# Kernel optimization log

Measured on AMD Instinct MI355X. Metric: run time of the kernel, lower is better.

The kernel has to match this reference:

```python
import jax, jax.numpy as jnp
import numpy as np

DIM = 128
N = 8192
E = 262144
EPS = 1e-8  # torch.cosine_similarity eps


def setup_inputs() -> dict:
    key = jax.random.key(0)
    k1, k2, k3, k4 = jax.random.split(key, 4)
    x = jax.random.normal(k1, (N, DIM), dtype=jnp.float32)
    edge_index = jax.random.randint(k2, (2, E), 0, N, dtype=jnp.int32)
    # GCNConv parameters: linear weight (glorot-ish) and bias
    W_gcn = jax.random.normal(k3, (DIM, DIM), dtype=jnp.float32) / np.sqrt(DIM)
    b_gcn = jnp.zeros((DIM,), dtype=jnp.float32)
    return {"x": x, "edge_index": edge_index, "W_gcn": W_gcn, "b_gcn": b_gcn}


def _cosine_attention(x):
    # torch.cosine_similarity(x.unsqueeze(1), x.unsqueeze(0), dim=-1)
    # == (x @ x.T) / max(||x_i|| * ||x_j||, eps)
    nrm = jnp.sqrt(jnp.sum(x * x, axis=-1))                      # [N]
    denom = jnp.maximum(nrm[:, None] * nrm[None, :], EPS)        # [N, N]
    sim = (x @ x.T) / denom                                      # [N, N]
    return jax.nn.sigmoid(sim @ x)                               # [N, dim]


def _gcn_conv(x, edge_index, W, b):
    n = x.shape[0]
    xw = x @ W                                                   # [N, dim]
    # add self-loops
    loops = jnp.arange(n, dtype=edge_index.dtype)
    row = jnp.concatenate([edge_index[0], loops])                # source
    col = jnp.concatenate([edge_index[1], loops])                # target
    # symmetric normalization: deg computed on target nodes
    deg = jax.ops.segment_sum(jnp.ones_like(col, dtype=x.dtype), col, num_segments=n)
    dis = jnp.where(deg > 0, jax.lax.rsqrt(jnp.maximum(deg, 1.0)), 0.0)
    dis = jnp.where(deg > 0, deg ** -0.5, 0.0)
    norm = dis[row] * dis[col]                                   # [E+N]
    msgs = xw[row] * norm[:, None]                               # [E+N, dim]
    out = jax.ops.segment_sum(msgs, col, num_segments=n)         # [N, dim]
    return out + b


def reference(x, edge_index, W_gcn, b_gcn):
    att = _cosine_attention(x)
    g = _gcn_conv(x, edge_index, W_gcn, b_gcn)
    return g * att
```

## Files before the change

### kernel.cpp

```cpp
#include <hip/hip_runtime.h>
#include <math.h>

#define NN   8192
#define DIM  128
#define NE   262144
#define XB   128
#define HB   64
#define EPB  (NE / HB)
#define RWB  32
#define BK   16
#define SMEMF (64 * DIM + 64)

static __device__ __forceinline__ unsigned short f2bf(float f) {
  unsigned int u = __float_as_uint(f);
  return (unsigned short)((u + 0x7FFFu + ((u >> 16) & 1u)) >> 16);
}
static __device__ __forceinline__ float bf2f(unsigned short h) {
  return __uint_as_float((unsigned int)h << 16);
}


static __device__ void ph_xtx(int u, int tid, float* smem,
    const float* __restrict__ x, float* __restrict__ rinv,
    float* __restrict__ Mpart) {
  float* xs  = smem;
  float* rvs = smem + 64 * DIM;
  int row0 = u * 64;
  const float4* xsrc = (const float4*)(x + (size_t)row0 * DIM);
  float4* xdst = (float4*)xs;
  #pragma unroll
  for (int i = 0; i < 8; ++i) xdst[tid + 256 * i] = xsrc[tid + 256 * i];
  __syncthreads();
  int rr = tid >> 2, q = tid & 3;
  const float4* xr = (const float4*)&xs[rr * DIM + q * 32];
  float ss = 0.f;
  #pragma unroll
  for (int i = 0; i < 8; ++i) {
    float4 v = xr[i];
    ss += v.x * v.x + v.y * v.y + v.z * v.z + v.w * v.w;
  }
  ss += __shfl_xor(ss, 1);
  ss += __shfl_xor(ss, 2);
  if (q == 0) { float rv = 1.0f / sqrtf(ss); rvs[rr] = rv; rinv[row0 + rr] = rv; }
  __syncthreads();

  int ty = tid >> 4, tx = tid & 15;
  float acc[8][8];
  #pragma unroll
  for (int i = 0; i < 8; ++i)
    #pragma unroll
    for (int j = 0; j < 8; ++j) acc[i][j] = 0.f;
  #pragma unroll 2
  for (int r = 0; r < 64; ++r) {
    float4 a0 = *(const float4*)&xs[r * DIM + ty * 8];
    float4 a1 = *(const float4*)&xs[r * DIM + ty * 8 + 4];
    float4 b0 = *(const float4*)&xs[r * DIM + tx * 8];
    float4 b1 = *(const float4*)&xs[r * DIM + tx * 8 + 4];
    float rv = rvs[r];
    float a[8] = {a0.x * rv, a0.y * rv, a0.z * rv, a0.w * rv,
                  a1.x * rv, a1.y * rv, a1.z * rv, a1.w * rv};
    float b[8] = {b0.x, b0.y, b0.z, b0.w, b1.x, b1.y, b1.z, b1.w};
    #pragma unroll
    for (int i = 0; i < 8; ++i)
      #pragma unroll
      for (int j = 0; j < 8; ++j) acc[i][j] += a[i] * b[j];
  }
  float* o = Mpart + (size_t)u * (DIM * DIM);
  #pragma unroll
  for (int i = 0; i < 8; ++i) {
    *(float4*)&o[(ty * 8 + i) * DIM + tx * 8]     = make_float4(acc[i][0], acc[i][1], acc[i][2], acc[i][3]);
    *(float4*)&o[(ty * 8 + i) * DIM + tx * 8 + 4] = make_float4(acc[i][4], acc[i][5], acc[i][6], acc[i][7]);
  }
}

static __device__ void ph_hist(int h, int tid, int* ldeg,
    const int* __restrict__ ei, int* __restrict__ gcnt, int* __restrict__ slot) {
  int4* lz = (int4*)ldeg;
  #pragma unroll
  for (int i = tid; i < NN / 4; i += 256) lz[i] = make_int4(0, 0, 0, 0);
  __syncthreads();
  int e0 = h * EPB + tid * 16;
  int4 c0 = *(const int4*)(ei + NE + e0);
  int4 c1 = *(const int4*)(ei + NE + e0 + 4);
  int4 c2 = *(const int4*)(ei + NE + e0 + 8);
  int4 c3 = *(const int4*)(ei + NE + e0 + 12);
  int r0  = atomicAdd(&ldeg[c0.x], 1);
  int r1  = atomicAdd(&ldeg[c0.y], 1);
  int r2  = atomicAdd(&ldeg[c0.z], 1);
  int r3  = atomicAdd(&ldeg[c0.w], 1);
  int r4  = atomicAdd(&ldeg[c1.x], 1);
  int r5  = atomicAdd(&ldeg[c1.y], 1);
  int r6  = atomicAdd(&ldeg[c1.z], 1);
  int r7  = atomicAdd(&ldeg[c1.w], 1);
  int r8  = atomicAdd(&ldeg[c2.x], 1);
  int r9  = atomicAdd(&ldeg[c2.y], 1);
  int r10 = atomicAdd(&ldeg[c2.z], 1);
  int r11 = atomicAdd(&ldeg[c2.w], 1);
  int r12 = atomicAdd(&ldeg[c3.x], 1);
  int r13 = atomicAdd(&ldeg[c3.y], 1);
  int r14 = atomicAdd(&ldeg[c3.z], 1);
  int r15 = atomicAdd(&ldeg[c3.w], 1);
  __syncthreads();
  int binb = tid * 32;
  #pragma unroll
  for (int i = 0; i < 8; ++i) {
    int4 v = *(int4*)&ldeg[binb + i * 4];
    if (v.x) ldeg[binb + i * 4 + 0] = atomicAdd(&gcnt[binb + i * 4 + 0], v.x);
    if (v.y) ldeg[binb + i * 4 + 1] = atomicAdd(&gcnt[binb + i * 4 + 1], v.y);
    if (v.z) ldeg[binb + i * 4 + 2] = atomicAdd(&gcnt[binb + i * 4 + 2], v.z);
    if (v.w) ldeg[binb + i * 4 + 3] = atomicAdd(&gcnt[binb + i * 4 + 3], v.w);
  }
  __syncthreads();
  int4 s0 = make_int4(ldeg[c0.x] + r0,  ldeg[c0.y] + r1,  ldeg[c0.z] + r2,  ldeg[c0.w] + r3);
  int4 s1 = make_int4(ldeg[c1.x] + r4,  ldeg[c1.y] + r5,  ldeg[c1.z] + r6,  ldeg[c1.w] + r7);
  int4 s2 = make_int4(ldeg[c2.x] + r8,  ldeg[c2.y] + r9,  ldeg[c2.z] + r10, ldeg[c2.w] + r11);
  int4 s3 = make_int4(ldeg[c3.x] + r12, ldeg[c3.y] + r13, ldeg[c3.z] + r14, ldeg[c3.w] + r15);
  *(int4*)(slot + e0)      = s0;
  *(int4*)(slot + e0 + 4)  = s1;
  *(int4*)(slot + e0 + 8)  = s2;
  *(int4*)(slot + e0 + 12) = s3;
}

static __device__ void ph_mred(int u, int tid, float* smem,
    const float* __restrict__ Mpart, float* __restrict__ Mmat) {
  int j0 = u * 64;
  int jj = tid & 63, sub = tid >> 6;
  const float* mp = Mpart + (size_t)(sub * 32) * (DIM * DIM) + j0;
  float s = 0.f;
  #pragma unroll 4
  for (int k = 0; k < 32; ++k) s += mp[(size_t)k * (DIM * DIM) + jj];
  smem[sub * 64 + jj] = s;
  __syncthreads();
  if (tid < 64)
    Mmat[j0 + tid] = smem[tid] + smem[64 + tid] + smem[128 + tid] + smem[192 + tid];
}

static __device__ void ph_scan(int tid, int* wsum,
    const int* __restrict__ gcnt, int* __restrict__ offs, float* __restrict__ dis) {
  int lane = tid & 63, wave = tid >> 6;
  const int4* g4 = (const int4*)gcnt;
  int s = 0;
  #pragma unroll
  for (int i = 0; i < 8; ++i) { int4 v = g4[tid * 8 + i]; s += v.x + v.y + v.z + v.w; }
  int sc = s;
  #pragma unroll
  for (int off = 1; off < 64; off <<= 1) {
    int v = __shfl_up(sc, off);
    if (lane >= off) sc += v;
  }
  if (lane == 63) wsum[wave] = sc;
  __syncthreads();
  if (wave == 0 && lane < 4) {
    int v = wsum[lane];
    #pragma unroll
    for (int off = 1; off < 4; off <<= 1) {
      int u = __shfl_up(v, off);
      if (lane >= off) v += u;
    }
    wsum[lane] = v;
  }
  __syncthreads();
  int run = (wave ? wsum[wave - 1] : 0) + sc - s;
  #pragma unroll
  for (int i = 0; i < 8; ++i) {
    int4 v = g4[tid * 8 + i];
    int4 o;
    o.x = run; run += v.x;
    o.y = run; run += v.y;
    o.z = run; run += v.z;
    o.w = run; run += v.w;
    *(int4*)&offs[tid * 32 + i * 4] = o;
    float4 d;
    d.x = rsqrtf((float)(v.x + 1)); d.y = rsqrtf((float)(v.y + 1));
    d.z = rsqrtf((float)(v.z + 1)); d.w = rsqrtf((float)(v.w + 1));
    *(float4*)&dis[tid * 32 + i * 4] = d;
  }
}

static __device__ void ph_gemm(int u, int tid, float* smem,
    const float* __restrict__ x, const float* __restrict__ W,
    const float* __restrict__ Mmat, const float* __restrict__ rinv,
    const float* __restrict__ dis, unsigned short* __restrict__ xws,
    float* __restrict__ att) {
  float* xs  = smem;
  float* Wl  = smem + 4096;
  float* Ml  = smem + 6144;
  float* rvs = smem + 8192;
  float* dss = smem + 8224;
  int row0 = u * RWB;
  const float4* xsrc = (const float4*)(x + (size_t)row0 * DIM);
  float4* xdst = (float4*)xs;
  #pragma unroll
  for (int i = 0; i < 4; ++i) xdst[tid + 256 * i] = xsrc[tid + 256 * i];
  if (tid < RWB) { rvs[tid] = rinv[row0 + tid]; dss[tid] = dis[row0 + tid]; }

  int ty = tid >> 5, tx = tid & 31;
  int r0 = ty * 4;
  float4 aw[4], am[4];
  #pragma unroll
  for (int j = 0; j < 4; ++j) { aw[j] = make_float4(0,0,0,0); am[j] = make_float4(0,0,0,0); }

  for (int kk = 0; kk < DIM; kk += BK) {
    __syncthreads();
    const float4* Ws = (const float4*)(W + (size_t)kk * DIM);
    const float4* Ms = (const float4*)(Mmat + (size_t)kk * DIM);
    float4 w0s = Ws[tid], w1s = Ws[tid + 256];
    float4 m0s = Ms[tid], m1s = Ms[tid + 256];
    ((float4*)Wl)[tid]       = w0s;
    ((float4*)Wl)[tid + 256] = w1s;
    ((float4*)Ml)[tid]       = m0s;
    ((float4*)Ml)[tid + 256] = m1s;
    __syncthreads();
    #pragma unroll
    for (int k4 = 0; k4 < BK; k4 += 4) {
      float4 xf[4];
      #pragma unroll
      for (int j = 0; j < 4; ++j)
        xf[j] = *(const float4*)&xs[(r0 + j) * DIM + kk + k4];
      #pragma unroll
      for (int k = 0; k < 4; ++k) {
        float4 wv = *(const float4*)&Wl[(k4 + k) * DIM + tx * 4];
        float4 mv = *(const float4*)&Ml[(k4 + k) * DIM + tx * 4];
        #pragma unroll
        for (int j = 0; j < 4; ++j) {
          float xv = ((const float*)&xf[j])[k];
          aw[j].x += xv * wv.x; aw[j].y += xv * wv.y;
          aw[j].z += xv * wv.z; aw[j].w += xv * wv.w;
          am[j].x += xv * mv.x; am[j].y += xv * mv.y;
          am[j].z += xv * mv.z; am[j].w += xv * mv.w;
        }
      }
    }
  }
  #pragma unroll
  for (int j = 0; j < 4; ++j) {
    int row = row0 + r0 + j;
    float rv = rvs[r0 + j], ds = dss[r0 + j];
    size_t o = (size_t)row * DIM + tx * 4;
    ushort4 wb;
    wb.x = f2bf(aw[j].x * ds);
    wb.y = f2bf(aw[j].y * ds);
    wb.z = f2bf(aw[j].z * ds);
    wb.w = f2bf(aw[j].w * ds);
    *(ushort4*)&xws[o] = wb;
    float4 g;
    g.x = 1.0f / (1.0f + __expf(-am[j].x * rv));
    g.y = 1.0f / (1.0f + __expf(-am[j].y * rv));
    g.z = 1.0f / (1.0f + __expf(-am[j].z * rv));
    g.w = 1.0f / (1.0f + __expf(-am[j].w * rv));
    *(float4*)&att[o] = g;
  }
}

static __device__ void ph_place(int u, int tid,
    const int* __restrict__ ei, const int* __restrict__ offs,
    const int* __restrict__ slot, int* __restrict__ sorted) {
  int e0 = u * EPB + tid * 16;
  #pragma unroll
  for (int i = 0; i < 4; ++i) {
    int4 sv = *(const int4*)(ei + e0 + i * 4);
    int4 cv = *(const int4*)(ei + NE + e0 + i * 4);
    int4 sl = *(const int4*)(slot + e0 + i * 4);
    sorted[offs[cv.x] + sl.x] = sv.x;
    sorted[offs[cv.y] + sl.y] = sv.y;
    sorted[offs[cv.z] + sl.z] = sv.z;
    sorted[offs[cv.w] + sl.w] = sv.w;
  }
}

__global__ __launch_bounds__(256) void k_pA(const float* __restrict__ x,
    const int* __restrict__ ei, float* __restrict__ rinv,
    float* __restrict__ Mpart, int* __restrict__ gcnt, int* __restrict__ slot) {
  __shared__ float smem[SMEMF];
  int u = blockIdx.x, tid = threadIdx.x;
  if (u < XB) ph_xtx(u, tid, smem, x, rinv, Mpart);
  else        ph_hist(u - XB, tid, (int*)smem, ei, gcnt, slot);
}
__global__ __launch_bounds__(256) void k_pB(const float* __restrict__ Mpart,
    float* __restrict__ Mmat, const int* __restrict__ gcnt,
    int* __restrict__ offs, float* __restrict__ dis) {
  __shared__ float smem[SMEMF];
  int u = blockIdx.x, tid = threadIdx.x;
  if (u < 256) ph_mred(u, tid, smem, Mpart, Mmat);
  else         ph_scan(tid, (int*)smem, gcnt, offs, dis);
}
__global__ __launch_bounds__(256) void k_pC(const float* __restrict__ x,
    const float* __restrict__ W, const float* __restrict__ Mmat,
    const float* __restrict__ rinv, const float* __restrict__ dis,
    const int* __restrict__ ei, const int* __restrict__ offs,
    const int* __restrict__ slot, int* __restrict__ sorted,
    unsigned short* __restrict__ xws, float* __restrict__ att) {
  __shared__ float smem[SMEMF];
  int u = blockIdx.x, tid = threadIdx.x;
  if (u < NN / RWB) ph_gemm(u, tid, smem, x, W, Mmat, rinv, dis, xws, att);
  else              ph_place(u - NN / RWB, tid, ei, offs, slot, sorted);
}
__global__ __launch_bounds__(128) void k_pD(const int* __restrict__ offs,
    const int* __restrict__ gcnt, const float* __restrict__ dis,
    const unsigned short* __restrict__ xws, const float* __restrict__ att,
    const float* __restrict__ bias, const int* __restrict__ sorted,
    float* __restrict__ out) {
  int c = blockIdx.x, t = threadIdx.x;
  int base = offs[c];
  int cnt  = gcnt[c];
  float acc = bf2f(xws[(size_t)c * DIM + t]);
  int k = 0;
  for (; k + 4 <= cnt; k += 4) {
    int s0 = sorted[base + k + 0];
    int s1 = sorted[base + k + 1];
    int s2 = sorted[base + k + 2];
    int s3 = sorted[base + k + 3];
    float v0 = bf2f(xws[(size_t)s0 * DIM + t]);
    float v1 = bf2f(xws[(size_t)s1 * DIM + t]);
    float v2 = bf2f(xws[(size_t)s2 * DIM + t]);
    float v3 = bf2f(xws[(size_t)s3 * DIM + t]);
    acc += v0 + v1 + v2 + v3;
  }
  for (; k < cnt; ++k)
    acc += bf2f(xws[(size_t)sorted[base + k] * DIM + t]);
  float g = acc * dis[c] + bias[t];
  out[(size_t)c * DIM + t] = g * att[(size_t)c * DIM + t];
}

extern "C" void kernel_launch(void* const* d_in, const int* in_sizes, int n_in,
                              void* d_out, int out_size, void* d_ws, size_t ws_size,
                              hipStream_t stream) {
  const float* x  = (const float*)d_in[0];
  const int*   ei = (const int*)  d_in[1];
  const float* W  = (const float*)d_in[2];
  const float* b  = (const float*)d_in[3];
  float* out = (float*)d_out;

  unsigned short* xws = (unsigned short*)d_ws;
  float* att   = (float*)(xws + (size_t)NN * DIM);
  float* Mpart = att + (size_t)NN * DIM;
  float* Mmat  = Mpart + (size_t)XB * DIM * DIM;
  float* rinv  = Mmat + DIM * DIM;
  float* dis   = rinv + NN;
  int*   gcnt  = (int*)(dis + NN);
  int*   offs  = gcnt + NN;
  int*   slot  = offs + NN;
  int*   sorted= slot + NE;

  hipMemsetAsync(gcnt, 0, NN * sizeof(int), stream);

  k_pA<<<XB + HB, 256, 0, stream>>>(x, ei, rinv, Mpart, gcnt, slot);
  k_pB<<<257, 256, 0, stream>>>(Mpart, Mmat, gcnt, offs, dis);
  k_pC<<<NN / RWB + HB, 256, 0, stream>>>(x, W, Mmat, rinv, dis, ei, offs,
                                          slot, sorted, xws, att);
  k_pD<<<NN, 128, 0, stream>>>(offs, gcnt, dis, xws, att, b, sorted, out);
}
```

Measured before the change: 117.5 us.

## Rework GEMM thread tiling, pad smem, and vectorize bf16 gather in aggregation

The Gram-matrix phase switches to a split-half column mapping that cuts LDS bank conflicts. The fused GEMM now runs 128 threads per block, each holding an 8-column tile, and stores x in padded shared memory. The place phase uses more, smaller blocks. The aggregation kernel drops to 64 threads per node and reads two bf16 values per 32-bit load, with int4 index loads and an 8-way unroll. Together these aim to raise memory efficiency and ILP in the gather-heavy final kernel, at the cost of fewer threads per block and more registers.

Result: no change. 116.4 us (-0.9%).

```diff
diff --git a/kernel.cpp b/kernel.cpp
--- a/kernel.cpp
+++ b/kernel.cpp
@@ -5,18 +5,21 @@
 #define DIM  128
 #define NE   262144
 #define XB   128
-#define HB   64
-#define EPB  (NE / HB)
+#define HBH  64
+#define HEB  (NE / HBH)
+#define PBP  128
+#define PEB  (NE / PBP)
 #define RWB  32
 #define BK   16
-#define SMEMF (64 * DIM + 64)
+#define XSS  132
+#define SMEMF 8448
 
 static __device__ __forceinline__ unsigned short f2bf(float f) {
   unsigned int u = __float_as_uint(f);
   return (unsigned short)((u + 0x7FFFu + ((u >> 16) & 1u)) >> 16);
 }
-static __device__ __forceinline__ float bf2f(unsigned short h) {
-  return __uint_as_float((unsigned int)h << 16);
+static __device__ __forceinline__ float bf2f(unsigned int h) {
+  return __uint_as_float(h << 16);
 }
 
 
@@ -52,10 +55,10 @@
     for (int j = 0; j < 8; ++j) acc[i][j] = 0.f;
   #pragma unroll 2
   for (int r = 0; r < 64; ++r) {
-    float4 a0 = *(const float4*)&xs[r * DIM + ty * 8];
-    float4 a1 = *(const float4*)&xs[r * DIM + ty * 8 + 4];
-    float4 b0 = *(const float4*)&xs[r * DIM + tx * 8];
-    float4 b1 = *(const float4*)&xs[r * DIM + tx * 8 + 4];
+    float4 a0 = *(const float4*)&xs[r * DIM + ty * 4];
+    float4 a1 = *(const float4*)&xs[r * DIM + 64 + ty * 4];
+    float4 b0 = *(const float4*)&xs[r * DIM + tx * 4];
+    float4 b1 = *(const float4*)&xs[r * DIM + 64 + tx * 4];
     float rv = rvs[r];
     float a[8] = {a0.x * rv, a0.y * rv, a0.z * rv, a0.w * rv,
                   a1.x * rv, a1.y * rv, a1.z * rv, a1.w * rv};
@@ -68,8 +71,9 @@
   float* o = Mpart + (size_t)u * (DIM * DIM);
   #pragma unroll
   for (int i = 0; i < 8; ++i) {
-    *(float4*)&o[(ty * 8 + i) * DIM + tx * 8]     = make_float4(acc[i][0], acc[i][1], acc[i][2], acc[i][3]);
-    *(float4*)&o[(ty * 8 + i) * DIM + tx * 8 + 4] = make_float4(acc[i][4], acc[i][5], acc[i][6], acc[i][7]);
+    int row = (i < 4) ? (ty * 4 + i) : (64 + ty * 4 + (i - 4));
+    *(float4*)&o[row * DIM + tx * 4]      = make_float4(acc[i][0], acc[i][1], acc[i][2], acc[i][3]);
+    *(float4*)&o[row * DIM + 64 + tx * 4] = make_float4(acc[i][4], acc[i][5], acc[i][6], acc[i][7]);
   }
 }
 
@@ -79,7 +83,7 @@
   #pragma unroll
   for (int i = tid; i < NN / 4; i += 256) lz[i] = make_int4(0, 0, 0, 0);
   __syncthreads();
-  int e0 = h * EPB + tid * 16;
+  int e0 = h * HEB + tid * 16;
   int4 c0 = *(const int4*)(ei + NE + e0);
   int4 c1 = *(const int4*)(ei + NE + e0 + 4);
   int4 c2 = *(const int4*)(ei + NE + e0 + 8);
@@ -183,51 +187,62 @@
     const float* __restrict__ dis, unsigned short* __restrict__ xws,
     float* __restrict__ att) {
   float* xs  = smem;
-  float* Wl  = smem + 4096;
-  float* Ml  = smem + 6144;
-  float* rvs = smem + 8192;
-  float* dss = smem + 8224;
+  float* Wl  = smem + 4224;
+  float* Ml  = smem + 6272;
+  float* rvs = smem + 8320;
+  float* dss = smem + 8352;
   int row0 = u * RWB;
-  const float4* xsrc = (const float4*)(x + (size_t)row0 * DIM);
-  float4* xdst = (float4*)xs;
-  #pragma unroll
-  for (int i = 0; i < 4; ++i) xdst[tid + 256 * i] = xsrc[tid + 256 * i];
+  #pragma unroll
+  for (int i = 0; i < 8; ++i) {
+    int fidx = i * 128 + tid;
+    int row = fidx >> 5, c4 = fidx & 31;
+    ((float4*)(xs + row * XSS))[c4] =
+        ((const float4*)(x + (size_t)(row0 + row) * DIM))[c4];
+  }
   if (tid < RWB) { rvs[tid] = rinv[row0 + tid]; dss[tid] = dis[row0 + tid]; }
 
-  int ty = tid >> 5, tx = tid & 31;
-  int r0 = ty * 4;
-  float4 aw[4], am[4];
-  #pragma unroll
-  for (int j = 0; j < 4; ++j) { aw[j] = make_float4(0,0,0,0); am[j] = make_float4(0,0,0,0); }
+  int ry = tid >> 4, tx = tid & 15;
+  int r0 = ry * 4;
+  float4 aw0[4], aw1[4], am0[4], am1[4];
+  #pragma unroll
+  for (int j = 0; j < 4; ++j) {
+    aw0[j] = make_float4(0,0,0,0); aw1[j] = make_float4(0,0,0,0);
+    am0[j] = make_float4(0,0,0,0); am1[j] = make_float4(0,0,0,0);
+  }
 
   for (int kk = 0; kk < DIM; kk += BK) {
     __syncthreads();
     const float4* Ws = (const float4*)(W + (size_t)kk * DIM);
     const float4* Ms = (const float4*)(Mmat + (size_t)kk * DIM);
-    float4 w0s = Ws[tid], w1s = Ws[tid + 256];
-    float4 m0s = Ms[tid], m1s = Ms[tid + 256];
-    ((float4*)Wl)[tid]       = w0s;
-    ((float4*)Wl)[tid + 256] = w1s;
-    ((float4*)Ml)[tid]       = m0s;
-    ((float4*)Ml)[tid + 256] = m1s;
+    #pragma unroll
+    for (int i = 0; i < 4; ++i) {
+      ((float4*)Wl)[tid + 128 * i] = Ws[tid + 128 * i];
+      ((float4*)Ml)[tid + 128 * i] = Ms[tid + 128 * i];
+    }
     __syncthreads();
     #pragma unroll
     for (int k4 = 0; k4 < BK; k4 += 4) {
       float4 xf[4];
       #pragma unroll
       for (int j = 0; j < 4; ++j)
-        xf[j] = *(const float4*)&xs[(r0 + j) * DIM + kk + k4];
+        xf[j] = *(const float4*)&xs[(r0 + j) * XSS + kk + k4];
       #pragma unroll
       for (int k = 0; k < 4; ++k) {
-        float4 wv = *(const float4*)&Wl[(k4 + k) * DIM + tx * 4];
-        float4 mv = *(const float4*)&Ml[(k4 + k) * DIM + tx * 4];
+        float4 wv0 = *(const float4*)&Wl[(k4 + k) * DIM + tx * 4];
+        float4 wv1 = *(const float4*)&Wl[(k4 + k) * DIM + 64 + tx * 4];
+        float4 mv0 = *(const float4*)&Ml[(k4 + k) * DIM + tx * 4];
+        float4 mv1 = *(const float4*)&Ml[(k4 + k) * DIM + 64 + tx * 4];
         #pragma unroll
         for (int j = 0; j < 4; ++j) {
           float xv = ((const float*)&xf[j])[k];
-          aw[j].x += xv * wv.x; aw[j].y += xv * wv.y;
-          aw[j].z += xv * wv.z; aw[j].w += xv * wv.w;
-          am[j].x += xv * mv.x; am[j].y += xv * mv.y;
-          am[j].z += xv * mv.z; am[j].w += xv * mv.w;
+          aw0[j].x += xv * wv0.x; aw0[j].y += xv * wv0.y;
+          aw0[j].z += xv * wv0.z; aw0[j].w += xv * wv0.w;
+          aw1[j].x += xv * wv1.x; aw1[j].y += xv * wv1.y;
+          aw1[j].z += xv * wv1.z; aw1[j].w += xv * wv1.w;
+          am0[j].x += xv * mv0.x; am0[j].y += xv * mv0.y;
+          am0[j].z += xv * mv0.z; am0[j].w += xv * mv0.w;
+          am1[j].x += xv * mv1.x; am1[j].y += xv * mv1.y;
+          am1[j].z += xv * mv1.z; am1[j].w += xv * mv1.w;
         }
       }
     }
@@ -236,26 +251,33 @@
   for (int j = 0; j < 4; ++j) {
     int row = row0 + r0 + j;
     float rv = rvs[r0 + j], ds = dss[r0 + j];
-    size_t o = (size_t)row * DIM + tx * 4;
-    ushort4 wb;
-    wb.x = f2bf(aw[j].x * ds);
-    wb.y = f2bf(aw[j].y * ds);
-    wb.z = f2bf(aw[j].z * ds);
-    wb.w = f2bf(aw[j].w * ds);
-    *(ushort4*)&xws[o] = wb;
-    float4 g;
-    g.x = 1.0f / (1.0f + __expf(-am[j].x * rv));
-    g.y = 1.0f / (1.0f + __expf(-am[j].y * rv));
-    g.z = 1.0f / (1.0f + __expf(-am[j].z * rv));
-    g.w = 1.0f / (1.0f + __expf(-am[j].w * rv));
-    *(float4*)&att[o] = g;
+    size_t oA = (size_t)row * DIM + tx * 4;
+    size_t oB = oA + 64;
+    ushort4 wbA, wbB;
+    wbA.x = f2bf(aw0[j].x * ds); wbA.y = f2bf(aw0[j].y * ds);
+    wbA.z = f2bf(aw0[j].z * ds); wbA.w = f2bf(aw0[j].w * ds);
+    wbB.x = f2bf(aw1[j].x * ds); wbB.y = f2bf(aw1[j].y * ds);
+    wbB.z = f2bf(aw1[j].z * ds); wbB.w = f2bf(aw1[j].w * ds);
+    *(ushort4*)&xws[oA] = wbA;
+    *(ushort4*)&xws[oB] = wbB;
+    float4 gA, gB;
+    gA.x = 1.0f / (1.0f + __expf(-am0[j].x * rv));
+    gA.y = 1.0f / (1.0f + __expf(-am0[j].y * rv));
+    gA.z = 1.0f / (1.0f + __expf(-am0[j].z * rv));
+    gA.w = 1.0f / (1.0f + __expf(-am0[j].w * rv));
+    gB.x = 1.0f / (1.0f + __expf(-am1[j].x * rv));
+    gB.y = 1.0f / (1.0f + __expf(-am1[j].y * rv));
+    gB.z = 1.0f / (1.0f + __expf(-am1[j].z * rv));
+    gB.w = 1.0f / (1.0f + __expf(-am1[j].w * rv));
+    *(float4*)&att[oA] = gA;
+    *(float4*)&att[oB] = gB;
   }
 }
 
 static __device__ void ph_place(int u, int tid,
     const int* __restrict__ ei, const int* __restrict__ offs,
     const int* __restrict__ slot, int* __restrict__ sorted) {
-  int e0 = u * EPB + tid * 16;
+  int e0 = u * PEB + tid * 16;
   #pragma unroll
   for (int i = 0; i < 4; ++i) {
     int4 sv = *(const int4*)(ei + e0 + i * 4);
@@ -284,7 +306,7 @@
   if (u < 256) ph_mred(u, tid, smem, Mpart, Mmat);
   else         ph_scan(tid, (int*)smem, gcnt, offs, dis);
 }
-__global__ __launch_bounds__(256) void k_pC(const float* __restrict__ x,
+__global__ __launch_bounds__(128) void k_pC(const float* __restrict__ x,
     const float* __restrict__ W, const float* __restrict__ Mmat,
     const float* __restrict__ rinv, const float* __restrict__ dis,
     const int* __restrict__ ei, const int* __restrict__ offs,
@@ -295,7 +317,7 @@
   if (u < NN / RWB) ph_gemm(u, tid, smem, x, W, Mmat, rinv, dis, xws, att);
   else              ph_place(u - NN / RWB, tid, ei, offs, slot, sorted);
 }
-__global__ __launch_bounds__(128) void k_pD(const int* __restrict__ offs,
+__global__ __launch_bounds__(64) void k_pD(const int* __restrict__ offs,
     const int* __restrict__ gcnt, const float* __restrict__ dis,
     const unsigned short* __restrict__ xws, const float* __restrict__ att,
     const float* __restrict__ bias, const int* __restrict__ sorted,
@@ -303,23 +325,47 @@
   int c = blockIdx.x, t = threadIdx.x;
   int base = offs[c];
   int cnt  = gcnt[c];
-  float acc = bf2f(xws[(size_t)c * DIM + t]);
+  const unsigned int* xw2 = (const unsigned int*)xws;
+  unsigned int sv = xw2[(size_t)c * 64 + t];
+  float acc0 = bf2f(sv & 0xffffu), acc1 = bf2f(sv >> 16);
   int k = 0;
+  for (; k + 8 <= cnt; k += 8) {
+    int4 i0 = *(const int4*)(sorted + base + k);
+    int4 i1 = *(const int4*)(sorted + base + k + 4);
+    unsigned int v0 = xw2[(size_t)i0.x * 64 + t];
+    unsigned int v1 = xw2[(size_t)i0.y * 64 + t];
+    unsigned int v2 = xw2[(size_t)i0.z * 64 + t];
+    unsigned int v3 = xw2[(size_t)i0.w * 64 + t];
+    unsigned int v4 = xw2[(size_t)i1.x * 64 + t];
+    unsigned int v5 = xw2[(size_t)i1.y * 64 + t];
+    unsigned int v6 = xw2[(size_t)i1.z * 64 + t];
+    unsigned int v7 = xw2[(size_t)i1.w * 64 + t];
+    acc0 += bf2f(v0 & 0xffffu) + bf2f(v1 & 0xffffu) + bf2f(v2 & 0xffffu) + bf2f(v3 & 0xffffu)
+          + bf2f(v4 & 0xffffu) + bf2f(v5 & 0xffffu) + bf2f(v6 & 0xffffu) + bf2f(v7 & 0xffffu);
+    acc1 += bf2f(v0 >> 16) + bf2f(v1 >> 16) + bf2f(v2 >> 16) + bf2f(v3 >> 16)
+          + bf2f(v4 >> 16) + bf2f(v5 >> 16) + bf2f(v6 >> 16) + bf2f(v7 >> 16);
+  }
   for (; k + 4 <= cnt; k += 4) {
-    int s0 = sorted[base + k + 0];
-    int s1 = sorted[base + k + 1];
-    int s2 = sorted[base + k + 2];
-    int s3 = sorted[base + k + 3];
-    float v0 = bf2f(xws[(size_t)s0 * DIM + t]);
-    float v1 = bf2f(xws[(size_t)s1 * DIM + t]);
-    float v2 = bf2f(xws[(size_t)s2 * DIM + t]);
-    float v3 = bf2f(xws[(size_t)s3 * DIM + t]);
-    acc += v0 + v1 + v2 + v3;
-  }
-  for (; k < cnt; ++k)
-    acc += bf2f(xws[(size_t)sorted[base + k] * DIM + t]);
-  float g = acc * dis[c] + bias[t];
-  out[(size_t)c * DIM + t] = g * att[(size_t)c * DIM + t];
+    int4 i0 = *(const int4*)(sorted + base + k);
+    unsigned int v0 = xw2[(size_t)i0.x * 64 + t];
+    unsigned int v1 = xw2[(size_t)i0.y * 64 + t];
+    unsigned int v2 = xw2[(size_t)i0.z * 64 + t];
+    unsigned int v3 = xw2[(size_t)i0.w * 64 + t];
+    acc0 += bf2f(v0 & 0xffffu) + bf2f(v1 & 0xffffu) + bf2f(v2 & 0xffffu) + bf2f(v3 & 0xffffu);
+    acc1 += bf2f(v0 >> 16) + bf2f(v1 >> 16) + bf2f(v2 >> 16) + bf2f(v3 >> 16);
+  }
+  for (; k < cnt; ++k) {
+    unsigned int v = xw2[(size_t)sorted[base + k] * 64 + t];
+    acc0 += bf2f(v & 0xffffu);
+    acc1 += bf2f(v >> 16);
+  }
+  float dc = dis[c];
+  float2 at = ((const float2*)att)[(size_t)c * 64 + t];
+  float2 bs = ((const float2*)bias)[t];
+  float2 o;
+  o.x = (acc0 * dc + bs.x) * at.x;
+  o.y = (acc1 * dc + bs.y) * at.y;
+  ((float2*)out)[(size_t)c * 64 + t] = o;
 }
 
 extern "C" void kernel_launch(void* const* d_in, const int* in_sizes, int n_in,
@@ -344,9 +390,9 @@
 
   hipMemsetAsync(gcnt, 0, NN * sizeof(int), stream);
 
-  k_pA<<<XB + HB, 256, 0, stream>>>(x, ei, rinv, Mpart, gcnt, slot);
+  k_pA<<<XB + HBH, 256, 0, stream>>>(x, ei, rinv, Mpart, gcnt, slot);
   k_pB<<<257, 256, 0, stream>>>(Mpart, Mmat, gcnt, offs, dis);
-  k_pC<<<NN / RWB + HB, 256, 0, stream>>>(x, W, Mmat, rinv, dis, ei, offs,
-                                          slot, sorted, xws, att);
-  k_pD<<<NN, 128, 0, stream>>>(offs, gcnt, dis, xws, att, b, sorted, out);
-}
+  k_pC<<<NN / RWB + PBP, 128, 0, stream>>>(x, W, Mmat, rinv, dis, ei, offs,
+                                           slot, sorted, xws, att);
+  k_pD<<<NN, 64, 0, stream>>>(offs, gcnt, dis, xws, att, b, sorted, out);
+}
```
